# Kernel tuning notes

Hardware: AMD Instinct MI355X
Metric: run time of the kernel (lower is better)

The kernel has to match this reference:

```python
import jax, jax.numpy as jnp
import numpy as np

ORDER = 32
ATAN_ALPHA = 2.0  # spikingjelly surrogate.ATan default


@jax.custom_vjp
def atan_spike(x):
    # Heaviside forward with ATan surrogate gradient (spikingjelly ATan)
    return (x >= 0).astype(x.dtype)

def _atan_fwd(x):
    return (x >= 0).astype(x.dtype), x

def _atan_bwd(x, g):
    s = (jnp.pi / 2.0) * ATAN_ALPHA * x
    return (g * (ATAN_ALPHA / 2.0) / (1.0 + s * s),)

atan_spike.defvjp(_atan_fwd, _atan_bwd)


def gen_gemm_weight(w, T):
    # W[i, j] = w[order-1 - (i-j)] if 0 <= i-j < order else 0 (banded lower Toeplitz)
    i = jnp.arange(T)[:, None]
    j = jnp.arange(T)[None, :]
    d = i - j
    idx = jnp.clip(ORDER - 1 - d, 0, ORDER - 1)
    return jnp.where((d >= 0) & (d < ORDER), w[idx], jnp.zeros((), w.dtype))


def setup_inputs() -> dict:
    key = jax.random.key(0)
    k1, = jax.random.split(key, 1)
    B, T, D = 16, 1024, 1024
    x_seq = jax.random.normal(k1, (B, T, D), dtype=jnp.float32)
    # exp_init: weight[order-1] = 1, weight[i] = weight[i+1] / 2
    weight = (2.0 ** jnp.arange(1 - ORDER, 1, dtype=jnp.float32))
    threshold = -jnp.ones((1,), dtype=jnp.float32)
    return {"x_seq": x_seq, "weight": weight, "threshold": threshold}


def reference(x_seq, weight, threshold):
    T = x_seq.shape[1]
    W = gen_gemm_weight(weight, T)                      # [T, T]
    # F.linear over the time axis: h[b,t,d] = sum_k W[t,k] x[b,k,d] + threshold
    h = jnp.einsum("tk,bkd->btd", W, x_seq) + threshold
    return atan_spike(h)
```

## Files before the change

kernel.cpp:

```cpp
#include <hip/hip_runtime.h>
#include <math.h>

#define ORDER 32
#define TC 16

__global__ __launch_bounds__(256)
void psn_kernel(const float2* __restrict__ x,
                const float* __restrict__ w,
                const float* __restrict__ thr_p,
                float2* __restrict__ out)
{
    const int T = 1024, D2 = 512;
    const int d2 = blockIdx.x * blockDim.x + threadIdx.x;
    const int t0 = blockIdx.y * TC;
    const int b  = blockIdx.z;

    const float thr = thr_p[0];
    const size_t base = (size_t)b * T * D2 + d2;
    const float2* xb = x + base;
    float2*       ob = out + base;

    float2 xv[TC + ORDER - 1];
    if (t0 >= ORDER - 1) {
        const float2* p = xb + (size_t)(t0 - (ORDER - 1)) * D2;
        #pragma unroll
        for (int i = 0; i < TC + ORDER - 1; ++i)
            xv[i] = p[(size_t)i * D2];
    } else {
        #pragma unroll
        for (int i = 0; i < TC + ORDER - 1; ++i) {
            const int t = t0 - (ORDER - 1) + i;
            if (t >= 0) xv[i] = xb[(size_t)t * D2];
            else        { xv[i].x = 0.0f; xv[i].y = 0.0f; }
        }
    }

    #pragma unroll
    for (int tt = 0; tt < TC; ++tt) {
        float hx = thr, hy = thr;
        #pragma unroll
        for (int j = 0; j < ORDER; ++j) {
            const float wj = w[j];
            hx = fmaf(wj, xv[tt + j].x, hx);
            hy = fmaf(wj, xv[tt + j].y, hy);
        }

        float rx, ry;
        if (__builtin_expect(fabsf(hx) < 1e-3f || fabsf(hy) < 1e-3f, 0)) {
            double dx = (double)thr, dy = (double)thr;
            #pragma unroll
            for (int j = 0; j < ORDER; ++j) {
                dx = fma((double)w[j], (double)xv[tt + j].x, dx);
                dy = fma((double)w[j], (double)xv[tt + j].y, dy);
            }
            rx = (dx >= 0.0) ? 1.0f : 0.0f;
            ry = (dy >= 0.0) ? 1.0f : 0.0f;
        } else {
            rx = (hx >= 0.0f) ? 1.0f : 0.0f;
            ry = (hy >= 0.0f) ? 1.0f : 0.0f;
        }
        float2 r; r.x = rx; r.y = ry;
        ob[(size_t)(t0 + tt) * D2] = r;
    }
}

extern "C" void kernel_launch(void* const* d_in, const int* in_sizes, int n_in,
                              void* d_out, int out_size, void* d_ws, size_t ws_size,
                              hipStream_t stream)
{
    const float2* x  = (const float2*)d_in[0];
    const float* w   = (const float*)d_in[1];
    const float* thr = (const float*)d_in[2];
    float2* o = (float2*)d_out;

    dim3 grid(512 / 256, 1024 / TC, 16);
    psn_kernel<<<grid, 256, 0, stream>>>(x, w, thr, o);
}
```

Measured before the change: 135.9 us.

## Use float4 loads, fewer timesteps per thread, and nontemporal stores

Widens per-thread accesses from float2 to float4 along D and cuts the time rows each thread computes from 16 to 8. Threads are regrouped into 512-thread blocks where 8 wavefronts cover consecutive time chunks of the same 64-column slice. Output uses nontemporal stores to keep the write stream out of the cache. The halo overhead rises, since each thread loads 39 rows to produce 8 instead of 47 for 16, which adds more redundant reads and more registers per thread.

New measurement: 259.1 us. +90.7%, slower.

```diff
diff --git a/kernel.cpp b/kernel.cpp
--- a/kernel.cpp
+++ b/kernel.cpp
@@ -2,65 +2,81 @@
 #include <math.h>
 
 #define ORDER 32
-#define TC 16
+#define T_DIM 1024
+#define D4 256
+#define TCB 64
+#define RPT 8
 
-__global__ __launch_bounds__(256)
-void psn_kernel(const float2* __restrict__ x,
+typedef float f32x4 __attribute__((ext_vector_type(4)));
+
+__global__ __launch_bounds__(512)
+void psn_kernel(const f32x4* __restrict__ x,
                 const float* __restrict__ w,
                 const float* __restrict__ thr_p,
-                float2* __restrict__ out)
+                f32x4* __restrict__ out)
 {
-    const int T = 1024, D2 = 512;
-    const int d2 = blockIdx.x * blockDim.x + threadIdx.x;
-    const int t0 = blockIdx.y * TC;
-    const int b  = blockIdx.z;
+    const int d4     = blockIdx.x * 64 + (threadIdx.x & 63);
+    const int tg     = threadIdx.x >> 6;
+    const int t_base = blockIdx.y * TCB + tg * RPT;
+    const int b      = blockIdx.z;
 
     const float thr = thr_p[0];
-    const size_t base = (size_t)b * T * D2 + d2;
-    const float2* xb = x + base;
-    float2*       ob = out + base;
+    const size_t base = (size_t)b * T_DIM * D4 + d4;
+    const f32x4* xb = x + base;
+    f32x4*       ob = out + base;
 
-    float2 xv[TC + ORDER - 1];
-    if (t0 >= ORDER - 1) {
-        const float2* p = xb + (size_t)(t0 - (ORDER - 1)) * D2;
+    f32x4 xv[RPT + ORDER - 1];
+    if (t_base >= ORDER - 1) {
+        const f32x4* p = xb + (size_t)(t_base - (ORDER - 1)) * D4;
         #pragma unroll
-        for (int i = 0; i < TC + ORDER - 1; ++i)
-            xv[i] = p[(size_t)i * D2];
+        for (int i = 0; i < RPT + ORDER - 1; ++i)
+            xv[i] = p[(size_t)i * D4];
     } else {
         #pragma unroll
-        for (int i = 0; i < TC + ORDER - 1; ++i) {
-            const int t = t0 - (ORDER - 1) + i;
-            if (t >= 0) xv[i] = xb[(size_t)t * D2];
-            else        { xv[i].x = 0.0f; xv[i].y = 0.0f; }
+        for (int i = 0; i < RPT + ORDER - 1; ++i) {
+            const int t = t_base - (ORDER - 1) + i;
+            if (t >= 0) xv[i] = xb[(size_t)t * D4];
+            else        xv[i] = (f32x4){0.0f, 0.0f, 0.0f, 0.0f};
         }
     }
 
     #pragma unroll
-    for (int tt = 0; tt < TC; ++tt) {
-        float hx = thr, hy = thr;
+    for (int r = 0; r < RPT; ++r) {
+        f32x4 h = {thr, thr, thr, thr};
         #pragma unroll
         for (int j = 0; j < ORDER; ++j) {
             const float wj = w[j];
-            hx = fmaf(wj, xv[tt + j].x, hx);
-            hy = fmaf(wj, xv[tt + j].y, hy);
+            h[0] = fmaf(wj, xv[r + j][0], h[0]);
+            h[1] = fmaf(wj, xv[r + j][1], h[1]);
+            h[2] = fmaf(wj, xv[r + j][2], h[2]);
+            h[3] = fmaf(wj, xv[r + j][3], h[3]);
         }
 
-        float rx, ry;
-        if (__builtin_expect(fabsf(hx) < 1e-3f || fabsf(hy) < 1e-3f, 0)) {
-            double dx = (double)thr, dy = (double)thr;
+        f32x4 res;
+        const bool near0 = (fabsf(h[0]) < 1e-3f) | (fabsf(h[1]) < 1e-3f) |
+                           (fabsf(h[2]) < 1e-3f) | (fabsf(h[3]) < 1e-3f);
+        if (__builtin_expect(near0, 0)) {
+            double d0 = (double)thr, d1 = (double)thr,
+                   d2 = (double)thr, d3 = (double)thr;
             #pragma unroll
             for (int j = 0; j < ORDER; ++j) {
-                dx = fma((double)w[j], (double)xv[tt + j].x, dx);
-                dy = fma((double)w[j], (double)xv[tt + j].y, dy);
+                const double wj = (double)w[j];
+                d0 = fma(wj, (double)xv[r + j][0], d0);
+                d1 = fma(wj, (double)xv[r + j][1], d1);
+                d2 = fma(wj, (double)xv[r + j][2], d2);
+                d3 = fma(wj, (double)xv[r + j][3], d3);
             }
-            rx = (dx >= 0.0) ? 1.0f : 0.0f;
-            ry = (dy >= 0.0) ? 1.0f : 0.0f;
+            res[0] = (d0 >= 0.0) ? 1.0f : 0.0f;
+            res[1] = (d1 >= 0.0) ? 1.0f : 0.0f;
+            res[2] = (d2 >= 0.0) ? 1.0f : 0.0f;
+            res[3] = (d3 >= 0.0) ? 1.0f : 0.0f;
         } else {
-            rx = (hx >= 0.0f) ? 1.0f : 0.0f;
-            ry = (hy >= 0.0f) ? 1.0f : 0.0f;
+            res[0] = (h[0] >= 0.0f) ? 1.0f : 0.0f;
+            res[1] = (h[1] >= 0.0f) ? 1.0f : 0.0f;
+            res[2] = (h[2] >= 0.0f) ? 1.0f : 0.0f;
+            res[3] = (h[3] >= 0.0f) ? 1.0f : 0.0f;
         }
-        float2 r; r.x = rx; r.y = ry;
-        ob[(size_t)(t0 + tt) * D2] = r;
+        __builtin_nontemporal_store(res, &ob[(size_t)(t_base + r) * D4]);
     }
 }
 
@@ -68,11 +84,11 @@
                               void* d_out, int out_size, void* d_ws, size_t ws_size,
                               hipStream_t stream)
 {
-    const float2* x  = (const float2*)d_in[0];
+    const f32x4* x   = (const f32x4*)d_in[0];
     const float* w   = (const float*)d_in[1];
     const float* thr = (const float*)d_in[2];
-    float2* o = (float2*)d_out;
+    f32x4* o = (f32x4*)d_out;
 
-    dim3 grid(512 / 256, 1024 / TC, 16);
-    psn_kernel<<<grid, 256, 0, stream>>>(x, w, thr, o);
+    dim3 grid(4, T_DIM / TCB, 16);
+    psn_kernel<<<grid, 512, 0, stream>>>(x, w, thr, o);
 }
```
